# Kernel tuning notes

Hardware: AMD Instinct MI355X
Metric: run time of the kernel (lower is better)

The kernel has to match this reference:

```python
import jax, jax.numpy as jnp
import numpy as np

B, L, D, H = 4, 2048, 2048, 16
HEAD_DIM = D // H
EPS = 1e-5


def rmsnorm(x, w):
    # fp32 RMSNorm as in the torch module
    xf = x.astype(jnp.float32)
    rms = jnp.sqrt(jnp.mean(xf * xf, axis=-1, keepdims=True) + EPS)
    return xf / rms * w


def apply_rope(x, freqs):
    # x: (..., D) with interleaved even/odd pairs; freqs: (2, L, D/2) = (sin, cos)
    sin, cos = freqs[0], freqs[1]
    xr = x.reshape(*x.shape[:-1], D // 2, 2)
    x_even, x_odd = xr[..., 0], xr[..., 1]
    e = x_even * cos - x_odd * sin
    o = x_odd * cos + x_even * sin
    return jnp.stack([e, o], axis=-1).reshape(x.shape)


def setup_inputs() -> dict:
    key = jax.random.key(0)
    k0, k1, k2 = jax.random.split(key, 3)
    x_BLD = jax.random.normal(k0, (B, L, D), dtype=jnp.float32)
    # realistic RoPE angle table over the full dim (matches module usage)
    t = jnp.arange(L, dtype=jnp.float32)[:, None]
    inv_freq = 1.0 / (10000.0 ** (jnp.arange(D // 2, dtype=jnp.float32) / (D // 2)))
    ang = t * inv_freq[None, :]                      # (L, D/2)
    freqs = jnp.stack([jnp.sin(ang), jnp.cos(ang)])  # (2, L, D/2)
    wqkv = jax.random.normal(k1, (3 * D, D), dtype=jnp.float32) * 0.02
    wo = jax.random.normal(k2, (D, D), dtype=jnp.float32) * 0.02
    q_norm_w = jnp.ones((D,), dtype=jnp.float32)
    k_norm_w = jnp.ones((D,), dtype=jnp.float32)
    return {"x_BLD": x_BLD, "freqs": freqs, "wqkv": wqkv, "wo": wo,
            "q_norm_w": q_norm_w, "k_norm_w": k_norm_w}


def reference(x_BLD, freqs, wqkv, wo, q_norm_w, k_norm_w):
    dtype = x_BLD.dtype
    qkv = x_BLD @ wqkv.T                             # (B, L, 3D)
    q, k, v = jnp.split(qkv, 3, axis=-1)
    q = apply_rope(rmsnorm(q, q_norm_w), freqs).astype(dtype)
    k = apply_rope(rmsnorm(k, k_norm_w), freqs).astype(dtype)
    # (B, L, D) -> (B, H, L, hd)
    q = q.reshape(B, L, H, HEAD_DIM).transpose(0, 2, 1, 3)
    k = k.reshape(B, L, H, HEAD_DIM).transpose(0, 2, 1, 3)
    v = v.reshape(B, L, H, HEAD_DIM).transpose(0, 2, 1, 3)
    scale = HEAD_DIM ** -0.5
    scores = jnp.einsum('bhqd,bhkd->bhqk', q, k) * scale
    attn = jax.nn.softmax(scores, axis=-1)
    out = jnp.einsum('bhqk,bhkd->bhqd', attn, v)
    out = out.transpose(0, 2, 1, 3).reshape(B, L, D)
    return out @ wo.T
```

## Files before the change

kernel.cpp:

```cpp
#include <hip/hip_runtime.h>
#include <stdint.h>
#include <stddef.h>

typedef unsigned short u16;
typedef __bf16 bf16x8 __attribute__((ext_vector_type(8)));
typedef __bf16 bf16x2 __attribute__((ext_vector_type(2)));
typedef float  f32x4  __attribute__((ext_vector_type(4)));
typedef float  f32x16 __attribute__((ext_vector_type(16)));

__device__ __forceinline__ float bf2f(u16 u){ return __uint_as_float(((unsigned)u)<<16); }
__device__ __forceinline__ u16 f2bf(float f){
  unsigned u = __float_as_uint(f);
  return (u16)((u + 0x7fffu + ((u>>16)&1u)) >> 16);
}
__device__ __forceinline__ void gl_lds16(const void* g, void* s){
  __builtin_amdgcn_global_load_lds(
      (__attribute__((address_space(1))) void*)(void*)g,
      (__attribute__((address_space(3))) void*)s, 16, 0, 0);
}

__global__ void k_f2bf(const float* __restrict__ in, u16* __restrict__ out, int n4){
  int i = blockIdx.x*256 + threadIdx.x;
  if (i < n4){
    float4 v = ((const float4*)in)[i];
    ((ushort4*)out)[i] = make_ushort4(f2bf(v.x), f2bf(v.y), f2bf(v.z), f2bf(v.w));
  }
}

#define BAR()  do{ __asm__ __volatile__("" ::: "memory"); \
                   __builtin_amdgcn_s_barrier(); \
                   __asm__ __volatile__("" ::: "memory"); }while(0)
#define VMC4()  __asm__ __volatile__("s_waitcnt vmcnt(4)" ::: "memory")
#define VMC0()  __asm__ __volatile__("s_waitcnt vmcnt(0)" ::: "memory")

#define STAGE_A(B_,H_,T_) do{ \
  const u16* _s = A + (size_t)(m0 + (H_)*128 + w16 + sr)*K + (T_)*64 + sc; \
  gl_lds16(_s,               &As[B_][H_][w16*64]); \
  gl_lds16(_s + (size_t)8*K, &As[B_][H_][(w16+8)*64]); }while(0)
#define STAGE_B(B_,H_,T_) do{ \
  const u16* _s = Bm + (size_t)(n0 + (H_)*128 + w16 + sr)*K + (T_)*64 + sc; \
  gl_lds16(_s,               &Bs[B_][H_][w16*64]); \
  gl_lds16(_s + (size_t)8*K, &Bs[B_][H_][(w16+8)*64]); }while(0)

#define RD_A(H_,B_) do{ \
  _Pragma("unroll") for (int mt=0; mt<4; ++mt){ \
    int r_ = wm*64 + mt*16 + l16; const u16* p_ = &As[B_][H_][r_*64]; \
    af[mt][0] = *(const bf16x8*)&p_[(( quad    ^ (r_&7))<<3)]; \
    af[mt][1] = *(const bf16x8*)&p_[(((quad+4) ^ (r_&7))<<3)]; } }while(0)
#define RD_B(H_,B_) do{ \
  _Pragma("unroll") for (int nt=0; nt<2; ++nt){ \
    int r_ = wn*32 + nt*16 + l16; const u16* p_ = &Bs[B_][H_][r_*64]; \
    bfr[nt][0] = *(const bf16x8*)&p_[(( quad    ^ (r_&7))<<3)]; \
    bfr[nt][1] = *(const bf16x8*)&p_[(((quad+4) ^ (r_&7))<<3)]; } }while(0)

#define MM(QM,QN) do{ \
  __builtin_amdgcn_sched_barrier(0); \
  __builtin_amdgcn_s_setprio(1); \
  _Pragma("unroll") for (int k_=0;k_<2;++k_) \
    _Pragma("unroll") for (int mt=0;mt<4;++mt) \
      _Pragma("unroll") for (int nt=0;nt<2;++nt) \
        acc[QM][QN][mt][nt] = __builtin_amdgcn_mfma_f32_16x16x32_bf16( \
            af[mt][k_], bfr[nt][k_], acc[QM][QN][mt][nt], 0,0,0); \
  __builtin_amdgcn_s_setprio(0); \
  __builtin_amdgcn_sched_barrier(0); }while(0)

template<int BF16OUT>
__global__ __launch_bounds__(512,2) void k_gemm256(const u16* __restrict__ A,
                                                   const u16* __restrict__ Bm,
                                                   void* __restrict__ Cout,
                                                   int M, int N, int K){
  __shared__ __align__(16) u16 As[2][2][128*64];
  __shared__ __align__(16) u16 Bs[2][2][128*64];
  const int tid = threadIdx.x, w = tid>>6, ln = tid&63;
  const int l16 = ln&15, quad = ln>>4;
  const int wm = w&1, wn = w>>1;
  const int w16 = w*16, sr = ln>>3;
  const int sc = ((ln&7) ^ sr) << 3;
  const int nbx = N>>8;
  const int nwg = nbx*(M>>8);
  const int lid = blockIdx.y*nbx + blockIdx.x;
  const int swz = (lid&7)*(nwg>>3) + (lid>>3);
  const int m0 = (swz/nbx)<<8, n0 = (swz%nbx)<<8;

  f32x4 acc[2][2][4][2];
  #pragma unroll
  for (int a=0;a<2;++a)
    #pragma unroll
    for (int b=0;b<2;++b)
      #pragma unroll
      for (int c=0;c<4;++c)
        #pragma unroll
        for (int d=0;d<2;++d){ acc[a][b][c][d][0]=0.f; acc[a][b][c][d][1]=0.f;
                               acc[a][b][c][d][2]=0.f; acc[a][b][c][d][3]=0.f; }
  bf16x8 af[4][2], bfr[2][2];

  STAGE_A(0,0,0); STAGE_B(0,0,0); STAGE_A(0,1,0); STAGE_B(0,1,0);
  STAGE_B(1,0,1); STAGE_A(1,1,1);
  VMC4(); BAR();

  const int niter = K>>7;
  for (int j=0; j<niter-1; ++j){
    const int t1 = 2*j+1;
    RD_A(0,0); RD_B(0,0); STAGE_A(1,0,t1);   BAR(); MM(0,0);
    RD_A(1,0);            STAGE_B(1,1,t1);   BAR(); MM(1,0);
    RD_B(1,0);            STAGE_B(0,0,t1+1); BAR(); MM(1,1);
    RD_A(0,0);            STAGE_A(0,1,t1+1); BAR(); MM(0,1); VMC4(); BAR();
    RD_A(0,1); RD_B(0,1); STAGE_A(0,0,t1+1); BAR(); MM(0,0);
    RD_A(1,1);            STAGE_B(0,1,t1+1); BAR(); MM(1,0);
    RD_B(1,1);            STAGE_B(1,0,t1+2); BAR(); MM(1,1);
    RD_A(0,1);            STAGE_A(1,1,t1+2); BAR(); MM(0,1); VMC4(); BAR();
  }
  {
    const int T1 = 2*niter-1;
    RD_A(0,0); RD_B(0,0); STAGE_A(1,0,T1);   BAR(); MM(0,0);
    RD_A(1,0);            STAGE_B(1,1,T1);   BAR(); MM(1,0);
    RD_B(1,0);                               BAR(); MM(1,1);
    RD_A(0,0);                               BAR(); MM(0,1); VMC0(); BAR();
    RD_A(0,1); RD_B(0,1);                    BAR(); MM(0,0);
    RD_A(1,1);                               BAR(); MM(1,0);
    RD_B(1,1);                               BAR(); MM(1,1);
    RD_A(0,1);                               BAR(); MM(0,1);
  }
  #pragma unroll
  for (int qm=0;qm<2;++qm)
    #pragma unroll
    for (int qn=0;qn<2;++qn)
      #pragma unroll
      for (int mt=0;mt<4;++mt)
        #pragma unroll
        for (int nt=0;nt<2;++nt)
          #pragma unroll
          for (int jj=0;jj<4;++jj){
            int row = m0 + qm*128 + wm*64 + mt*16 + quad*4 + jj;
            int col = n0 + qn*128 + wn*32 + nt*16 + l16;
            if (BF16OUT) ((u16*)Cout)[(size_t)row*N + col] = f2bf(acc[qm][qn][mt][nt][jj]);
            else         ((float*)Cout)[(size_t)row*N + col] = acc[qm][qn][mt][nt][jj];
          }
}

__global__ void k_prep_qk(const u16* __restrict__ qkv, const float* __restrict__ freqs,
                          const float* __restrict__ qw, const float* __restrict__ kw,
                          u16* __restrict__ Qo, u16* __restrict__ Ko){
  const int row = blockIdx.x;
  const int b = row >> 11, l = row & 2047;
  const int tid = threadIdx.x;
  const u16* qr = qkv + (size_t)row*6144;
  float qe[4], qo[4], ke[4], ko_[4];
  float sq = 0.f, sk = 0.f;
  #pragma unroll
  for (int it=0; it<4; ++it){
    int p = tid + it*256;
    ushort2 q2 = ((const ushort2*)qr)[p];
    ushort2 k2 = ((const ushort2*)(qr+2048))[p];
    qe[it]=bf2f(q2.x); qo[it]=bf2f(q2.y);
    ke[it]=bf2f(k2.x); ko_[it]=bf2f(k2.y);
    sq += qe[it]*qe[it] + qo[it]*qo[it];
    sk += ke[it]*ke[it] + ko_[it]*ko_[it];
  }
  #pragma unroll
  for (int off=32; off; off>>=1){ sq += __shfl_xor(sq, off); sk += __shfl_xor(sk, off); }
  __shared__ float red[8];
  if ((tid&63)==0){ red[tid>>6]=sq; red[4+(tid>>6)]=sk; }
  __syncthreads();
  sq = red[0]+red[1]+red[2]+red[3];
  sk = red[4]+red[5]+red[6]+red[7];
  const float rq = rsqrtf(sq*(1.f/2048.f) + 1e-5f);
  const float rk = rsqrtf(sk*(1.f/2048.f) + 1e-5f);
  const float QS = 0.08838834764831845f * 1.4426950408889634f;
  #pragma unroll
  for (int it=0; it<4; ++it){
    int p = tid + it*256;
    float sn = freqs[(size_t)l*1024 + p];
    float cs = freqs[2097152 + (size_t)l*1024 + p];
    float2 w2q = ((const float2*)qw)[p];
    float2 w2k = ((const float2*)kw)[p];
    int h = p>>6, dd2 = p&63;
    size_t o = ((size_t)(b*16+h)*2048 + l)*64 + dd2;
    float a = qe[it]*rq*w2q.x, c = qo[it]*rq*w2q.y;
    ((ushort2*)Qo)[o] = make_ushort2(f2bf((a*cs - c*sn)*QS), f2bf((c*cs + a*sn)*QS));
    a = ke[it]*rk*w2k.x; c = ko_[it]*rk*w2k.y;
    ((ushort2*)Ko)[o] = make_ushort2(f2bf(a*cs - c*sn), f2bf(c*cs + a*sn));
  }
}

__global__ void k_prep_v(const u16* __restrict__ qkv, u16* __restrict__ Vt){
  const int lt = blockIdx.x, bh = blockIdx.y;
  const int b = bh>>4, h = bh&15;
  __shared__ u16 tile[64][136];
  const int tid = threadIdx.x;
  #pragma unroll
  for (int it=0; it<32; ++it){
    int idx = it*256 + tid;
    int lo = idx >> 7, dd = idx & 127;
    tile[lo][dd] = qkv[(size_t)(b*2048 + lt*64 + lo)*6144 + 4096 + h*128 + dd];
  }
  __syncthreads();
  #pragma unroll
  for (int it=0; it<32; ++it){
    int idx = it*256 + tid;
    int dd = idx >> 6, lo = idx & 63;
    Vt[((size_t)bh*128 + dd)*2048 + lt*64 + lo] = tile[lo][dd];
  }
}

__global__ __launch_bounds__(256,2) void k_flash(const u16* __restrict__ Q,
                                                 const u16* __restrict__ Kg,
                                                 const u16* __restrict__ Vt,
                                                 u16* __restrict__ O){
  __shared__ __align__(16) u16 Kt[128*136];
  __shared__ __align__(16) u16 Vs[128*136];
  const int qt = blockIdx.x, bh = blockIdx.y;
  const int tid = threadIdx.x, w = tid>>6, ln = tid&63;
  const int l31 = ln&31, hi = ln>>5;
  const int b = bh>>4, h = bh&15;
  const size_t qkbase = (size_t)bh*(2048*128);

  const int srow = tid>>4, scol = tid&15;
  const u16* kgp = Kg + qkbase + (size_t)srow*128 + scol*8;
  const u16* vgp = Vt + (size_t)bh*(128*2048) + (size_t)srow*2048 + scol*8;
  u16* kld = &Kt[srow*136 + scol*8];
  u16* vld = &Vs[srow*136 + scol*8];

  bf16x8 qf[8];
  {
    const u16* qp = Q + qkbase + (size_t)(qt*128 + w*32 + l31)*128 + hi*8;
    #pragma unroll
    for (int kk=0; kk<8; ++kk) qf[kk] = *(const bf16x8*)(qp + kk*16);
  }

  union U4 { unsigned u[4]; bf16x8 v; };
  U4 uones; uones.u[0]=0x3F803F80u; uones.u[1]=0x3F803F80u;
  uones.u[2]=0x3F803F80u; uones.u[3]=0x3F803F80u;
  const bf16x8 ones = uones.v;

  f32x16 o[4], o4;
  #pragma unroll
  for (int dt=0; dt<4; ++dt)
    #pragma unroll
    for (int r=0; r<16; ++r) o[dt][r] = 0.f;
  #pragma unroll
  for (int r=0; r<16; ++r) o4[r] = 0.f;

  bf16x8 kreg[8], vreg[8];
  #pragma unroll
  for (int it=0; it<8; ++it) kreg[it] = *(const bf16x8*)(kgp + (size_t)it*16*128);
  #pragma unroll
  for (int it=0; it<8; ++it) vreg[it] = *(const bf16x8*)(vgp + (size_t)it*16*2048);

  for (int kt=0; kt<16; ++kt){
    __syncthreads();
    #pragma unroll
    for (int it=0; it<8; ++it) *(bf16x8*)(kld + it*16*136) = kreg[it];
    #pragma unroll
    for (int it=0; it<8; ++it) *(bf16x8*)(vld + it*16*136) = vreg[it];
    __syncthreads();
    if (kt < 15){
      #pragma unroll
      for (int it=0; it<8; ++it)
        kreg[it] = *(const bf16x8*)(kgp + (size_t)(kt+1)*128*128 + (size_t)it*16*128);
      #pragma unroll
      for (int it=0; it<8; ++it)
        vreg[it] = *(const bf16x8*)(vgp + (kt+1)*128 + (size_t)it*16*2048);
    }
    f32x16 s[4];
    #pragma unroll
    for (int t=0;t<4;++t)
      #pragma unroll
      for (int r=0;r<16;++r) s[t][r] = 0.f;
    #pragma unroll
    for (int kk=0; kk<8; ++kk){
      #pragma unroll
      for (int t=0; t<4; ++t){
        bf16x8 a = *(const bf16x8*)&Kt[(t*32 + l31)*136 + kk*16 + hi*8];
        s[t] = __builtin_amdgcn_mfma_f32_32x32x16_bf16(a, qf[kk], s[t], 0,0,0);
      }
    }
    bf16x8 bfrag[8];
    #pragma unroll
    for (int t=0;t<4;++t){
      unsigned pk[4][2];
      #pragma unroll
      for (int g=0;g<4;++g){
        float p0 = exp2f(s[t][g*4+0]);
        float p1 = exp2f(s[t][g*4+1]);
        float p2 = exp2f(s[t][g*4+2]);
        float p3 = exp2f(s[t][g*4+3]);
        bf16x2 c01, c23;
        c01[0] = (__bf16)p0; c01[1] = (__bf16)p1;
        c23[0] = (__bf16)p2; c23[1] = (__bf16)p3;
        pk[g][0] = __builtin_bit_cast(unsigned, c01);
        pk[g][1] = __builtin_bit_cast(unsigned, c23);
      }
      auto r0 = __builtin_amdgcn_permlane32_swap((int)pk[0][0], (int)pk[1][0], false, false);
      auto r1 = __builtin_amdgcn_permlane32_swap((int)pk[0][1], (int)pk[1][1], false, false);
      auto r2 = __builtin_amdgcn_permlane32_swap((int)pk[2][0], (int)pk[3][0], false, false);
      auto r3 = __builtin_amdgcn_permlane32_swap((int)pk[2][1], (int)pk[3][1], false, false);
      U4 u0, u1;
      u0.u[0] = (unsigned)r0[0]; u0.u[1] = (unsigned)r1[0];
      u0.u[2] = (unsigned)r0[1]; u0.u[3] = (unsigned)r1[1];
      u1.u[0] = (unsigned)r2[0]; u1.u[1] = (unsigned)r3[0];
      u1.u[2] = (unsigned)r2[1]; u1.u[3] = (unsigned)r3[1];
      bfrag[t*2+0] = u0.v;
      bfrag[t*2+1] = u1.v;
    }
    #pragma unroll
    for (int kk=0; kk<8; ++kk){
      #pragma unroll
      for (int dt=0; dt<4; ++dt){
        bf16x8 a = *(const bf16x8*)&Vs[(dt*32 + l31)*136 + kk*16 + hi*8];
        o[dt] = __builtin_amdgcn_mfma_f32_32x32x16_bf16(a, bfrag[kk], o[dt], 0,0,0);
      }
      o4 = __builtin_amdgcn_mfma_f32_32x32x16_bf16(ones, bfrag[kk], o4, 0,0,0);
    }
  }
  const float inv = 1.f/o4[0];
  __syncthreads();
  #pragma unroll
  for (int dt=0;dt<4;++dt)
    #pragma unroll
    for (int g=0;g<4;++g)
      *(ushort4*)&Kt[(w*32+l31)*136 + dt*32 + g*8 + hi*4] =
        make_ushort4(f2bf(o[dt][g*4+0]*inv), f2bf(o[dt][g*4+1]*inv),
                     f2bf(o[dt][g*4+2]*inv), f2bf(o[dt][g*4+3]*inv));
  __syncthreads();
  #pragma unroll
  for (int it=0; it<8; ++it){
    int q = it*16 + srow;
    bf16x8 vv = *(const bf16x8*)&Kt[q*136 + scol*8];
    *(bf16x8*)&O[(size_t)(b*2048 + qt*128 + q)*2048 + h*128 + scol*8] = vv;
  }
}

extern "C" void kernel_launch(void* const* d_in, const int* in_sizes, int n_in,
                              void* d_out, int out_size, void* d_ws, size_t ws_size,
                              hipStream_t stream){
  const float* x     = (const float*)d_in[0];
  const float* freqs = (const float*)d_in[1];
  const float* wqkv  = (const float*)d_in[2];
  const float* wo    = (const float*)d_in[3];
  const float* qw    = (const float*)d_in[4];
  const float* kw    = (const float*)d_in[5];
  char* ws = (char*)d_ws;
  u16* xbf    = (u16*)(ws);
  u16* wqkvbf = (u16*)(ws + 33554432);
  u16* wobf   = (u16*)(ws + 58720256);
  u16* qkvbf  = (u16*)(ws + 67108864);
  u16* Qbf    = (u16*)(ws + 167772160);
  u16* Kbf    = (u16*)(ws + 201326592);
  u16* Vtbf   = (u16*)(ws + 234881024);
  u16* Abf    = qkvbf;
  float* out  = (float*)d_out;

  k_f2bf<<<16384,256,0,stream>>>(x,    xbf,    4194304);
  k_f2bf<<<12288,256,0,stream>>>(wqkv, wqkvbf, 3145728);
  k_f2bf<<< 4096,256,0,stream>>>(wo,   wobf,   1048576);
  k_gemm256<1><<<dim3(24,32),512,0,stream>>>(xbf, wqkvbf, qkvbf, 8192, 6144, 2048);
  k_prep_qk<<<8192,256,0,stream>>>(qkvbf, freqs, qw, kw, Qbf, Kbf);
  k_prep_v<<<dim3(32,64),256,0,stream>>>(qkvbf, Vtbf);
  k_flash<<<dim3(16,64),256,0,stream>>>(Qbf, Kbf, Vtbf, Abf);
  k_gemm256<0><<<dim3(8,32),512,0,stream>>>(Abf, wobf, out, 8192, 2048, 2048);
}
```

Before: 659.8 us.

## Restructure GEMM main loop to load full B tile once per K-step

The bf16 GEMM mainloop is reorganised. Each K-step now reads all eight B fragments once and streams A in four 32-row slices, instead of re-reading A and B fragments for four quadrant sub-GEMMs. The global-to-LDS staging order and wait count change to match (vmcnt 4 to 6), giving a single barrier schedule per half-tile. The aim is fewer LDS reads and barriers per MFMA, at the cost of holding more B registers and a different load/compute overlap pattern.

```diff
diff --git a/kernel.cpp b/kernel.cpp
--- a/kernel.cpp
+++ b/kernel.cpp
@@ -30,7 +30,7 @@
 #define BAR()  do{ __asm__ __volatile__("" ::: "memory"); \
                    __builtin_amdgcn_s_barrier(); \
                    __asm__ __volatile__("" ::: "memory"); }while(0)
-#define VMC4()  __asm__ __volatile__("s_waitcnt vmcnt(4)" ::: "memory")
+#define VMC6()  __asm__ __volatile__("s_waitcnt vmcnt(6)" ::: "memory")
 #define VMC0()  __asm__ __volatile__("s_waitcnt vmcnt(0)" ::: "memory")
 
 #define STAGE_A(B_,H_,T_) do{ \
@@ -42,27 +42,36 @@
   gl_lds16(_s,               &Bs[B_][H_][w16*64]); \
   gl_lds16(_s + (size_t)8*K, &Bs[B_][H_][(w16+8)*64]); }while(0)
 
-#define RD_A(H_,B_) do{ \
-  _Pragma("unroll") for (int mt=0; mt<4; ++mt){ \
-    int r_ = wm*64 + mt*16 + l16; const u16* p_ = &As[B_][H_][r_*64]; \
-    af[mt][0] = *(const bf16x8*)&p_[(( quad    ^ (r_&7))<<3)]; \
-    af[mt][1] = *(const bf16x8*)&p_[(((quad+4) ^ (r_&7))<<3)]; } }while(0)
-#define RD_B(H_,B_) do{ \
-  _Pragma("unroll") for (int nt=0; nt<2; ++nt){ \
-    int r_ = wn*32 + nt*16 + l16; const u16* p_ = &Bs[B_][H_][r_*64]; \
-    bfr[nt][0] = *(const bf16x8*)&p_[(( quad    ^ (r_&7))<<3)]; \
-    bfr[nt][1] = *(const bf16x8*)&p_[(((quad+4) ^ (r_&7))<<3)]; } }while(0)
-
-#define MM(QM,QN) do{ \
+#define RD_A2(P_,B_) do{ \
+  _Pragma("unroll") for (int i_=0; i_<2; ++i_){ \
+    int r_ = wm*64 + (2*((P_)&1)+i_)*16 + l16; \
+    const u16* p_ = &As[B_][(P_)>>1][r_*64]; \
+    af[i_][0] = *(const bf16x8*)&p_[(( quad    ^ (r_&7))<<3)]; \
+    af[i_][1] = *(const bf16x8*)&p_[(((quad+4) ^ (r_&7))<<3)]; } }while(0)
+#define RD_B8(B_) do{ \
+  _Pragma("unroll") for (int j_=0; j_<4; ++j_){ \
+    int r_ = wn*32 + (j_&1)*16 + l16; \
+    const u16* p_ = &Bs[B_][j_>>1][r_*64]; \
+    bfr[j_][0] = *(const bf16x8*)&p_[(( quad    ^ (r_&7))<<3)]; \
+    bfr[j_][1] = *(const bf16x8*)&p_[(((quad+4) ^ (r_&7))<<3)]; } }while(0)
+
+#define MM_P(P_) do{ \
   __builtin_amdgcn_sched_barrier(0); \
   __builtin_amdgcn_s_setprio(1); \
   _Pragma("unroll") for (int k_=0;k_<2;++k_) \
-    _Pragma("unroll") for (int mt=0;mt<4;++mt) \
-      _Pragma("unroll") for (int nt=0;nt<2;++nt) \
-        acc[QM][QN][mt][nt] = __builtin_amdgcn_mfma_f32_16x16x32_bf16( \
-            af[mt][k_], bfr[nt][k_], acc[QM][QN][mt][nt], 0,0,0); \
+    _Pragma("unroll") for (int i_=0;i_<2;++i_) \
+      _Pragma("unroll") for (int j_=0;j_<4;++j_) \
+        acc[P_][i_][j_] = __builtin_amdgcn_mfma_f32_16x16x32_bf16( \
+            af[i_][k_], bfr[j_][k_], acc[P_][i_][j_], 0,0,0); \
   __builtin_amdgcn_s_setprio(0); \
   __builtin_amdgcn_sched_barrier(0); }while(0)
+
+#define TILE(B_,X_,T_,S1_,S2_,S3_,VM_) do{ \
+  RD_A2(0,B_); RD_B8(B_);                                        BAR(); MM_P(0); \
+  RD_A2(1,B_); if(S1_){STAGE_A(X_,1,(T_)+1);}                    BAR(); MM_P(1); \
+  RD_A2(2,B_); if(S2_){STAGE_B(B_,0,(T_)+2);STAGE_B(B_,1,(T_)+2);} BAR(); MM_P(2); \
+  RD_A2(3,B_); if(S3_){STAGE_A(B_,0,(T_)+2);} VM_;               BAR(); MM_P(3); \
+}while(0)
 
 template<int BF16OUT>
 __global__ __launch_bounds__(512,2) void k_gemm256(const u16* __restrict__ A,
@@ -82,60 +91,44 @@
   const int swz = (lid&7)*(nwg>>3) + (lid>>3);
   const int m0 = (swz/nbx)<<8, n0 = (swz%nbx)<<8;
 
-  f32x4 acc[2][2][4][2];
-  #pragma unroll
-  for (int a=0;a<2;++a)
+  f32x4 acc[4][2][4];
+  #pragma unroll
+  for (int a=0;a<4;++a)
     #pragma unroll
     for (int b=0;b<2;++b)
       #pragma unroll
-      for (int c=0;c<4;++c)
+      for (int c=0;c<4;++c){ acc[a][b][c][0]=0.f; acc[a][b][c][1]=0.f;
+                             acc[a][b][c][2]=0.f; acc[a][b][c][3]=0.f; }
+  bf16x8 af[2][2], bfr[4][2];
+
+  STAGE_B(0,0,0); STAGE_B(0,1,0); STAGE_A(0,0,0); STAGE_A(0,1,0);
+  STAGE_B(1,0,1); STAGE_B(1,1,1); STAGE_A(1,0,1);
+  VMC6(); BAR();
+
+  const int niter = (K>>7) - 1;
+  for (int j=0; j<niter; ++j){
+    const int t0 = 2*j;
+    TILE(0,1,t0,   1,1,1, VMC6());
+    TILE(1,0,t0+1, 1,1,1, VMC6());
+  }
+  {
+    const int t0 = K>>6;
+    TILE(0,1,t0-2, 1,0,0, VMC0());
+    TILE(1,0,t0-1, 0,0,0, );
+  }
+  #pragma unroll
+  for (int p=0;p<4;++p)
+    #pragma unroll
+    for (int i=0;i<2;++i)
+      #pragma unroll
+      for (int jj=0;jj<4;++jj)
         #pragma unroll
-        for (int d=0;d<2;++d){ acc[a][b][c][d][0]=0.f; acc[a][b][c][d][1]=0.f;
-                               acc[a][b][c][d][2]=0.f; acc[a][b][c][d][3]=0.f; }
-  bf16x8 af[4][2], bfr[2][2];
-
-  STAGE_A(0,0,0); STAGE_B(0,0,0); STAGE_A(0,1,0); STAGE_B(0,1,0);
-  STAGE_B(1,0,1); STAGE_A(1,1,1);
-  VMC4(); BAR();
-
-  const int niter = K>>7;
-  for (int j=0; j<niter-1; ++j){
-    const int t1 = 2*j+1;
-    RD_A(0,0); RD_B(0,0); STAGE_A(1,0,t1);   BAR(); MM(0,0);
-    RD_A(1,0);            STAGE_B(1,1,t1);   BAR(); MM(1,0);
-    RD_B(1,0);            STAGE_B(0,0,t1+1); BAR(); MM(1,1);
-    RD_A(0,0);            STAGE_A(0,1,t1+1); BAR(); MM(0,1); VMC4(); BAR();
-    RD_A(0,1); RD_B(0,1); STAGE_A(0,0,t1+1); BAR(); MM(0,0);
-    RD_A(1,1);            STAGE_B(0,1,t1+1); BAR(); MM(1,0);
-    RD_B(1,1);            STAGE_B(1,0,t1+2); BAR(); MM(1,1);
-    RD_A(0,1);            STAGE_A(1,1,t1+2); BAR(); MM(0,1); VMC4(); BAR();
-  }
-  {
-    const int T1 = 2*niter-1;
-    RD_A(0,0); RD_B(0,0); STAGE_A(1,0,T1);   BAR(); MM(0,0);
-    RD_A(1,0);            STAGE_B(1,1,T1);   BAR(); MM(1,0);
-    RD_B(1,0);                               BAR(); MM(1,1);
-    RD_A(0,0);                               BAR(); MM(0,1); VMC0(); BAR();
-    RD_A(0,1); RD_B(0,1);                    BAR(); MM(0,0);
-    RD_A(1,1);                               BAR(); MM(1,0);
-    RD_B(1,1);                               BAR(); MM(1,1);
-    RD_A(0,1);                               BAR(); MM(0,1);
-  }
-  #pragma unroll
-  for (int qm=0;qm<2;++qm)
-    #pragma unroll
-    for (int qn=0;qn<2;++qn)
-      #pragma unroll
-      for (int mt=0;mt<4;++mt)
-        #pragma unroll
-        for (int nt=0;nt<2;++nt)
-          #pragma unroll
-          for (int jj=0;jj<4;++jj){
-            int row = m0 + qm*128 + wm*64 + mt*16 + quad*4 + jj;
-            int col = n0 + qn*128 + wn*32 + nt*16 + l16;
-            if (BF16OUT) ((u16*)Cout)[(size_t)row*N + col] = f2bf(acc[qm][qn][mt][nt][jj]);
-            else         ((float*)Cout)[(size_t)row*N + col] = acc[qm][qn][mt][nt][jj];
-          }
+        for (int r=0;r<4;++r){
+          int row = m0 + (p>>1)*128 + wm*64 + (2*(p&1)+i)*16 + quad*4 + r;
+          int col = n0 + (jj>>1)*128 + wn*32 + (jj&1)*16 + l16;
+          if (BF16OUT) ((u16*)Cout)[(size_t)row*N + col] = f2bf(acc[p][i][jj][r]);
+          else         ((float*)Cout)[(size_t)row*N + col] = acc[p][i][jj][r];
+        }
 }
 
 __global__ void k_prep_qk(const u16* __restrict__ qkv, const float* __restrict__ freqs,
```

New measurement: 643.8 us. -2.4%, faster.
